# Kernel optimization log

Measured on AMD Instinct MI355X. Metric: run time of the kernel, lower is better.

## Reference

```python
import jax, jax.numpy as jnp
import numpy as np

B, T, D, H = 64, 2048, 256, 256

def setup_inputs() -> dict:
    key = jax.random.key(0)
    k1, k2, k3 = jax.random.split(key, 3)
    x = jax.random.normal(k1, (B, T, D), dtype=jnp.float32)
    # scaled init so tanh doesn't saturate over long sequences
    Wxh = jax.random.normal(k2, (D, H), dtype=jnp.float32) / np.sqrt(D)
    Whh = jax.random.normal(k3, (H, H), dtype=jnp.float32) / np.sqrt(H)
    b = jnp.zeros((H,), dtype=jnp.float32)
    return {"x": x, "Wxh": Wxh, "Whh": Whh, "b": b}

def reference(x, Wxh, Whh, b):
    # Vanilla tanh RNN cell: h_t = tanh(x_t @ Wxh + h_{t-1} @ Whh + b).
    # memory is None in the original forward -> init_memory gives zeros.
    # Precompute the input projection for all timesteps in one big GEMM.
    xp = jnp.einsum('btd,dh->bth', x, Wxh) + b  # [B, T, H]
    h0 = jnp.zeros((x.shape[0], Whh.shape[0]), dtype=x.dtype)

    def step(h, xp_t):
        h_new = jnp.tanh(xp_t + h @ Whh)
        return h_new, h_new

    _, hs = jax.lax.scan(step, h0, jnp.swapaxes(xp, 0, 1))  # hs: [T, B, H]
    return jnp.swapaxes(hs, 0, 1)  # [B, T, H], matches torch.cat(hiddens, dim=1)
```

## Files before the change

kernel.cpp:

```cpp
#include <hip/hip_runtime.h>
#include <hip/hip_bf16.h>
#include <cstdint>
#include <cstddef>

#define B_ 64
#define T_ 2048
#define D_ 256
#define H_ 256

#define PM 128
#define PN 128
#define PK 32

__global__ __launch_bounds__(256) void proj_kernel(const float* __restrict__ x,
                                                   const float* __restrict__ Wxh,
                                                   const float* __restrict__ bias,
                                                   float* __restrict__ xp) {
    __shared__ float As[PK][PM + 4];
    __shared__ float Bs[PK][PN + 4];
    const int tid = threadIdx.x;
    const int M0 = blockIdx.x * PM;
    const int N0 = blockIdx.y * PN;
    const int tr = tid >> 4;
    const int tc = tid & 15;

    float acc[8][8];
#pragma unroll
    for (int i = 0; i < 8; ++i)
#pragma unroll
        for (int j = 0; j < 8; ++j) acc[i][j] = 0.f;

    const int fA = tid & 7;
    const int rA = tid >> 3;
    const int kB = tid >> 3;
    const int fB = tid & 7;

    for (int kt = 0; kt < D_; kt += PK) {
#pragma unroll
        for (int i = 0; i < 4; ++i) {
            const int r = rA + i * 32;
            const float4 v = *(const float4*)&x[(size_t)(M0 + r) * D_ + kt + fA * 4];
            As[fA * 4 + 0][r] = v.x;
            As[fA * 4 + 1][r] = v.y;
            As[fA * 4 + 2][r] = v.z;
            As[fA * 4 + 3][r] = v.w;
        }
#pragma unroll
        for (int i = 0; i < 4; ++i) {
            const int c4 = fB + i * 8;
            const float4 v = *(const float4*)&Wxh[(size_t)(kt + kB) * H_ + N0 + c4 * 4];
            *(float4*)&Bs[kB][c4 * 4] = v;
        }
        __syncthreads();
#pragma unroll
        for (int k = 0; k < PK; ++k) {
            float a[8], bv[8];
            *(float4*)&a[0] = *(const float4*)&As[k][tr * 8];
            *(float4*)&a[4] = *(const float4*)&As[k][tr * 8 + 4];
            *(float4*)&bv[0] = *(const float4*)&Bs[k][tc * 8];
            *(float4*)&bv[4] = *(const float4*)&Bs[k][tc * 8 + 4];
#pragma unroll
            for (int i = 0; i < 8; ++i)
#pragma unroll
                for (int j = 0; j < 8; ++j)
                    acc[i][j] = fmaf(a[i], bv[j], acc[i][j]);
        }
        __syncthreads();
    }

    float bb[8];
    *(float4*)&bb[0] = *(const float4*)&bias[N0 + tc * 8];
    *(float4*)&bb[4] = *(const float4*)&bias[N0 + tc * 8 + 4];
#pragma unroll
    for (int i = 0; i < 8; ++i) {
        const size_t row = (size_t)(M0 + tr * 8 + i);
        float o[8];
#pragma unroll
        for (int j = 0; j < 8; ++j) o[j] = acc[i][j] + bb[j];
        *(float4*)&xp[row * H_ + N0 + tc * 8] = *(float4*)&o[0];
        *(float4*)&xp[row * H_ + N0 + tc * 8 + 4] = *(float4*)&o[4];
    }
}

typedef float f32x8 __attribute__((ext_vector_type(8)));

__global__ __launch_bounds__(512, 2) void rnn_kernel(const float* __restrict__ Whh,
                                                     float* __restrict__ io) {
    __shared__ float h_lds[H_];
    __shared__ float part[8 * 260];

    const int tid = threadIdx.x;
    const int b = blockIdx.x;
    const int colg = tid & 31;
    const int p = tid >> 5;
    const int w = tid >> 6;
    const int lane = tid & 63;
    const int j0 = colg * 8;
    const int k0 = p * 16;

    const float* wbase = &Whh[(size_t)k0 * H_ + j0];
#define LDW(KK) f32x8 w##KK = *(const f32x8*)(wbase + KK * H_);
    LDW(0)  LDW(1)  LDW(2)  LDW(3)  LDW(4)  LDW(5)  LDW(6)  LDW(7)
    LDW(8)  LDW(9)  LDW(10) LDW(11) LDW(12) LDW(13) LDW(14) LDW(15)
#undef LDW

    float* row_base = io + (size_t)b * T_ * H_;
    float xp0 = 0.f, xp1 = 0.f;
    if (tid < H_) {
        h_lds[tid] = 0.f;
        xp0 = row_base[tid];
        xp1 = row_base[H_ + tid];
    }
    __syncthreads();

    for (int t = 0; t < T_; ++t) {
        float xp2 = 0.f;
        if (tid < H_ && (t + 2) < T_) xp2 = row_base[(size_t)(t + 2) * H_ + tid];

        const float4* h4 = (const float4*)h_lds;
        const float4 hv0 = h4[p * 4 + 0];
        const float4 hv1 = h4[p * 4 + 1];
        const float4 hv2 = h4[p * 4 + 2];
        const float4 hv3 = h4[p * 4 + 3];

        f32x8 acc = w0 * hv0.x;
        acc += w1  * hv0.y;  acc += w2  * hv0.z;  acc += w3  * hv0.w;
        acc += w4  * hv1.x;  acc += w5  * hv1.y;  acc += w6  * hv1.z;  acc += w7  * hv1.w;
        acc += w8  * hv2.x;  acc += w9  * hv2.y;  acc += w10 * hv2.z;  acc += w11 * hv2.w;
        acc += w12 * hv3.x;  acc += w13 * hv3.y;  acc += w14 * hv3.z;  acc += w15 * hv3.w;

        float folded[8];
#pragma unroll
        for (int c = 0; c < 8; ++c)
            folded[c] = acc[c] + __shfl_xor(acc[c], 32, 64);

        if (lane < 32) {
            float* dst = &part[w * 260 + colg * 4];
            *(float4*)dst         = make_float4(folded[0], folded[1], folded[2], folded[3]);
            *(float4*)(dst + 128) = make_float4(folded[4], folded[5], folded[6], folded[7]);
        }
        __syncthreads();

        if (tid < H_) {
            const int idx = ((tid & 4) << 5) + ((tid >> 3) << 2) + (tid & 3);
            float s = xp0;
#pragma unroll
            for (int ww = 0; ww < 8; ++ww) s += part[ww * 260 + idx];
            const float h = tanhf(s);
            h_lds[tid] = h;
            row_base[(size_t)t * H_ + tid] = h;
            xp0 = xp1;
            xp1 = xp2;
        }
        __syncthreads();
    }
}

extern "C" void kernel_launch(void* const* d_in, const int* in_sizes, int n_in,
                              void* d_out, int out_size, void* d_ws, size_t ws_size,
                              hipStream_t stream) {
    const float* x    = (const float*)d_in[0];
    const float* Wxh  = (const float*)d_in[1];
    const float* Whh  = (const float*)d_in[2];
    const float* bias = (const float*)d_in[3];
    float* out = (float*)d_out;

    dim3 pgrid((B_ * T_) / PM, H_ / PN);
    proj_kernel<<<pgrid, dim3(256), 0, stream>>>(x, Wxh, bias, out);
    rnn_kernel<<<dim3(B_), dim3(512), 0, stream>>>(Whh, out);
}
```

Measured before the change: 1.947 ms.

## Widen RNN recurrence to 1024 threads with 4-wide weight slices per lane

The recurrent kernel now uses 1024 threads per batch row. Each wave owns 16 rows of Whh and each lane holds a 16x4 weight slice in registers. Partial sums go to a 16-wave LDS buffer, and the final reduction is spread across all threads using strided LDS reads plus two xor shuffles, replacing the cross-half shuffle and the 256-thread serial 8-way sum. The intent is to shorten the per-timestep critical path by cutting per-thread FMA work and reduction depth. In exchange, each step's barriers now synchronise 16 waves instead of 8, and an empty asm statement keeps the weights pinned in VGPRs.

```diff
diff --git a/kernel.cpp b/kernel.cpp
--- a/kernel.cpp
+++ b/kernel.cpp
@@ -82,73 +82,69 @@
     }
 }
 
-typedef float f32x8 __attribute__((ext_vector_type(8)));
+typedef float f4 __attribute__((ext_vector_type(4)));
 
-__global__ __launch_bounds__(512, 2) void rnn_kernel(const float* __restrict__ Whh,
-                                                     float* __restrict__ io) {
+__global__ __launch_bounds__(1024) __attribute__((amdgpu_waves_per_eu(4, 4)))
+void rnn_kernel(const float* __restrict__ Whh, float* __restrict__ io) {
     __shared__ float h_lds[H_];
-    __shared__ float part[8 * 260];
+    __shared__ float part[16 * 264];
 
     const int tid = threadIdx.x;
     const int b = blockIdx.x;
-    const int colg = tid & 31;
-    const int p = tid >> 5;
     const int w = tid >> 6;
-    const int lane = tid & 63;
-    const int j0 = colg * 8;
-    const int k0 = p * 16;
+    const int l = tid & 63;
+    const int j0 = l * 4;
+    const int q = l & 3;
+    const int jj = w * 16 + (l >> 2);
 
-    const float* wbase = &Whh[(size_t)k0 * H_ + j0];
-#define LDW(KK) f32x8 w##KK = *(const f32x8*)(wbase + KK * H_);
+    const float* wb = &Whh[(size_t)(w * 16) * H_ + j0];
+#define LDW(K) f4 wv##K = *(const f4*)(wb + K * H_);
     LDW(0)  LDW(1)  LDW(2)  LDW(3)  LDW(4)  LDW(5)  LDW(6)  LDW(7)
     LDW(8)  LDW(9)  LDW(10) LDW(11) LDW(12) LDW(13) LDW(14) LDW(15)
 #undef LDW
 
     float* row_base = io + (size_t)b * T_ * H_;
     float xp0 = 0.f, xp1 = 0.f;
-    if (tid < H_) {
-        h_lds[tid] = 0.f;
-        xp0 = row_base[tid];
-        xp1 = row_base[H_ + tid];
+    if (q == 0) {
+        xp0 = row_base[jj];
+        xp1 = row_base[H_ + jj];
     }
+    if (tid < H_) h_lds[tid] = 0.f;
     __syncthreads();
 
     for (int t = 0; t < T_; ++t) {
         float xp2 = 0.f;
-        if (tid < H_ && (t + 2) < T_) xp2 = row_base[(size_t)(t + 2) * H_ + tid];
+        if (q == 0 && (t + 2) < T_) xp2 = row_base[(size_t)(t + 2) * H_ + jj];
 
-        const float4* h4 = (const float4*)h_lds;
-        const float4 hv0 = h4[p * 4 + 0];
-        const float4 hv1 = h4[p * 4 + 1];
-        const float4 hv2 = h4[p * 4 + 2];
-        const float4 hv3 = h4[p * 4 + 3];
+        asm volatile("" : "+v"(wv0), "+v"(wv1), "+v"(wv2),  "+v"(wv3),
+                          "+v"(wv4), "+v"(wv5), "+v"(wv6),  "+v"(wv7),
+                          "+v"(wv8), "+v"(wv9), "+v"(wv10), "+v"(wv11),
+                          "+v"(wv12), "+v"(wv13), "+v"(wv14), "+v"(wv15));
 
-        f32x8 acc = w0 * hv0.x;
-        acc += w1  * hv0.y;  acc += w2  * hv0.z;  acc += w3  * hv0.w;
-        acc += w4  * hv1.x;  acc += w5  * hv1.y;  acc += w6  * hv1.z;  acc += w7  * hv1.w;
-        acc += w8  * hv2.x;  acc += w9  * hv2.y;  acc += w10 * hv2.z;  acc += w11 * hv2.w;
-        acc += w12 * hv3.x;  acc += w13 * hv3.y;  acc += w14 * hv3.z;  acc += w15 * hv3.w;
+        const f4* h4 = (const f4*)h_lds;
+        const f4 ha = h4[w * 4 + 0];
+        const f4 hb = h4[w * 4 + 1];
+        const f4 hc = h4[w * 4 + 2];
+        const f4 hd = h4[w * 4 + 3];
 
-        float folded[8];
-#pragma unroll
-        for (int c = 0; c < 8; ++c)
-            folded[c] = acc[c] + __shfl_xor(acc[c], 32, 64);
+        f4 acc = wv0 * ha.x;
+        acc += wv1  * ha.y;  acc += wv2  * ha.z;  acc += wv3  * ha.w;
+        acc += wv4  * hb.x;  acc += wv5  * hb.y;  acc += wv6  * hb.z;  acc += wv7  * hb.w;
+        acc += wv8  * hc.x;  acc += wv9  * hc.y;  acc += wv10 * hc.z;  acc += wv11 * hc.w;
+        acc += wv12 * hd.x;  acc += wv13 * hd.y;  acc += wv14 * hd.z;  acc += wv15 * hd.w;
 
-        if (lane < 32) {
-            float* dst = &part[w * 260 + colg * 4];
-            *(float4*)dst         = make_float4(folded[0], folded[1], folded[2], folded[3]);
-            *(float4*)(dst + 128) = make_float4(folded[4], folded[5], folded[6], folded[7]);
-        }
+        *(f4*)&part[w * 264 + l * 4] = acc;
         __syncthreads();
 
-        if (tid < H_) {
-            const int idx = ((tid & 4) << 5) + ((tid >> 3) << 2) + (tid & 3);
-            float s = xp0;
+        float s = 0.f;
 #pragma unroll
-            for (int ww = 0; ww < 8; ++ww) s += part[ww * 260 + idx];
-            const float h = tanhf(s);
-            h_lds[tid] = h;
-            row_base[(size_t)t * H_ + tid] = h;
+        for (int r = 0; r < 4; ++r) s += part[(r * 4 + q) * 264 + jj];
+        s += __shfl_xor(s, 1, 64);
+        s += __shfl_xor(s, 2, 64);
+        if (q == 0) {
+            const float h = tanhf(s + xp0);
+            h_lds[jj] = h;
+            row_base[(size_t)t * H_ + jj] = h;
             xp0 = xp1;
             xp1 = xp2;
         }
@@ -167,5 +163,5 @@
 
     dim3 pgrid((B_ * T_) / PM, H_ / PN);
     proj_kernel<<<pgrid, dim3(256), 0, stream>>>(x, Wxh, bias, out);
-    rnn_kernel<<<dim3(B_), dim3(512), 0, stream>>>(Whh, out);
+    rnn_kernel<<<dim3(B_), dim3(1024), 0, stream>>>(Whh, out);
 }
```

After: 2.396 ms. 23.0% more time.
